# Performance work log

Hardware: AMD Instinct MI355X
Metric: run time of the kernel (lower is better)

## Reference

```python
import jax, jax.numpy as jnp
import numpy as np

B, C, H, W = 32, 256, 32, 32
IC, MC, OC = 64, 16, 256


def setup_inputs() -> dict:
    key = jax.random.key(0)
    k = jax.random.split(key, 7)
    s = 1.0 / np.sqrt(C)
    s2 = 1.0 / np.sqrt(IC * MC)
    return {
        "x": jax.random.normal(k[0], (B, C, H, W), dtype=jnp.float32),
        "info_w": jax.random.uniform(k[1], (IC, C), jnp.float32, -s, s),
        "info_b": jax.random.uniform(k[2], (IC,), jnp.float32, -s, s),
        "mask_w": jax.random.uniform(k[3], (MC, C), jnp.float32, -s, s),
        "mask_b": jax.random.uniform(k[4], (MC,), jnp.float32, -s, s),
        "out_w": jax.random.uniform(k[5], (OC, IC * MC), jnp.float32, -s2, s2),
        "out_b": jax.random.uniform(k[6], (OC,), jnp.float32, -s2, s2),
    }


def reference(x, info_w, info_b, mask_w, mask_b, out_w, out_b):
    # 1x1 convs are channel GEMMs
    info = jax.nn.relu(jnp.einsum('ic,bchw->bihw', info_w, x) + info_b[None, :, None, None])   # [B,IC,H,W]
    mask = jax.nn.sigmoid(jnp.einsum('mc,bchw->bmhw', mask_w, x) + mask_b[None, :, None, None])  # [B,MC,H,W]
    # outer product over channels; concat order = for m: info * mask[m] -> index m*IC + i
    expanded = (mask[:, :, None, :, :] * info[:, None, :, :, :]).reshape(x.shape[0], MC * IC, x.shape[2], x.shape[3])
    out = jax.nn.relu(jnp.einsum('oe,behw->bohw', out_w, expanded) + out_b[None, :, None, None])
    return out
```

## Files before the change

kernel.cpp:

```cpp
#include <hip/hip_runtime.h>


typedef short bf16x8 __attribute__((ext_vector_type(8)));
typedef float f32x4  __attribute__((ext_vector_type(4)));

#define C_   256
#define HW_  1024
#define IC_  64
#define MC_  16
#define OC_  256
#define PX_  64
#define K_   1024

__global__ __launch_bounds__(256)
void split_w(const float2* __restrict__ w2, uint4* __restrict__ dst)
{
    const int tid  = blockIdx.x * 256 + threadIdx.x;
    const int lane = tid & 63;
    const int mi   = (tid >> 6) & 1;
    const int pl   = (tid >> 7) & 1;
    const int t    = (tid >> 8) & 31;
    const int ob   = (tid >> 13) & 7;

    const int row = ob * 32 + mi * 16 + (lane & 15);
    const int kq  = t * 16 + (lane >> 4) * 4;
    const float2* src = w2 + (size_t)row * (K_ / 2) + kq;

    unsigned int o[4];
    #pragma unroll
    for (int j = 0; j < 4; ++j) {
        const float2 v = src[j];
        const unsigned int u0 = __float_as_uint(v.x);
        const unsigned int u1 = __float_as_uint(v.y);
        if (pl == 0) {
            o[j] = (u0 >> 16) | (u1 & 0xffff0000u);
        } else {
            const float r0 = v.x - __uint_as_float(u0 & 0xffff0000u);
            const float r1 = v.y - __uint_as_float(u1 & 0xffff0000u);
            o[j] = (__float_as_uint(r0) >> 16) | (__float_as_uint(r1) & 0xffff0000u);
        }
    }
    dst[tid] = make_uint4(o[0], o[1], o[2], o[3]);
}

__global__ __launch_bounds__(512, 2)
void mul_layer_kernel(const float* __restrict__ x,
                      const float* __restrict__ info_w,
                      const float* __restrict__ info_b,
                      const float* __restrict__ mask_w,
                      const float* __restrict__ mask_b,
                      const bf16x8* __restrict__ wfrag,
                      const float* __restrict__ out_b,
                      float* __restrict__ out)
{
    __shared__ unsigned short ib[2 * PX_ * IC_];
    __shared__ float mask_pk[MC_ * PX_];

    const int lane = threadIdx.x & 63;
    const int wv   = __builtin_amdgcn_readfirstlane(threadIdx.x >> 6);
    const int bimg = blockIdx.x >> 4;
    const int tile = blockIdx.x & 15;
    const int hw0  = tile * PX_;

    {
        const float* xp = x + (size_t)bimg * C_ * HW_ + hw0 + lane;
        float racc[8] = {0.f,0.f,0.f,0.f,0.f,0.f,0.f,0.f};
        float macc[2] = {0.f,0.f};

        #pragma unroll 1
        for (int c0 = 0; c0 < C_; c0 += 16) {
            float xa[16];
            #pragma unroll
            for (int j = 0; j < 16; ++j) xa[j] = xp[(size_t)(c0 + j) * HW_];
            #pragma unroll
            for (int r = 0; r < 8; ++r) {
                const float* wr_ = info_w + (wv * 8 + r) * C_ + c0;
                #pragma unroll
                for (int j = 0; j < 16; ++j) racc[r] = fmaf(wr_[j], xa[j], racc[r]);
            }
            #pragma unroll
            for (int r = 0; r < 2; ++r) {
                const float* wr_ = mask_w + (wv * 2 + r) * C_ + c0;
                #pragma unroll
                for (int j = 0; j < 16; ++j) macc[r] = fmaf(wr_[j], xa[j], macc[r]);
            }
        }

        unsigned int H[4], L[4];
        #pragma unroll
        for (int rp = 0; rp < 4; ++rp) {
            float v0 = racc[2*rp]   + info_b[wv*8 + 2*rp];
            float v1 = racc[2*rp+1] + info_b[wv*8 + 2*rp+1];
            v0 = v0 > 0.f ? v0 : 0.f;
            v1 = v1 > 0.f ? v1 : 0.f;
            const unsigned int u0 = __float_as_uint(v0);
            const unsigned int u1 = __float_as_uint(v1);
            H[rp] = (u0 >> 16) | (u1 & 0xffff0000u);
            const float r0 = v0 - __uint_as_float(u0 & 0xffff0000u);
            const float r1 = v1 - __uint_as_float(u1 & 0xffff0000u);
            L[rp] = (__float_as_uint(r0) >> 16) | (__float_as_uint(r1) & 0xffff0000u);
        }
        const int sidx = ((lane >> 4) * 2 + (wv >> 2)) * 512 + (wv & 3) * 128 + (lane & 15) * 8;
        *(uint4*)(ib + sidx)                  = make_uint4(H[0], H[1], H[2], H[3]);
        *(uint4*)(ib + (PX_ * IC_) + sidx)    = make_uint4(L[0], L[1], L[2], L[3]);

        #pragma unroll
        for (int r = 0; r < 2; ++r) {
            float z = macc[r] + mask_b[wv * 2 + r];
            mask_pk[(wv * 2 + r) * PX_ + lane] = 1.0f / (1.0f + expf(-z));
        }
    }
    __syncthreads();

    const int lr = lane & 15;
    const int lg = lane >> 4;

    const bf16x8* Bp = (const bf16x8*)((const char*)ib + lg * 256 + lr * 16);
    const float*  Mp = mask_pk + lr;
    const bf16x8* Ap = wfrag + (size_t)wv * 8192 + lane;

    f32x4 acc[2][4];
    #pragma unroll
    for (int mi = 0; mi < 2; ++mi)
        #pragma unroll
        for (int ni = 0; ni < 4; ++ni)
            acc[mi][ni] = (f32x4){0.f, 0.f, 0.f, 0.f};

    bf16x8 h0a, h0b, l0a, l0b, h1a, h1b, l1a, l1b;
    h0a = Ap[0];   h0b = Ap[64];
    l0a = Ap[128]; l0b = Ap[192];

    #pragma unroll 1
    for (int m = 0; m < MC_; ++m) {
        const int t1 = 2 * m + 1;
        h1a = Ap[t1 * 256];       h1b = Ap[t1 * 256 + 64];
        l1a = Ap[t1 * 256 + 128]; l1b = Ap[t1 * 256 + 192];

        f32x4 tmp[2][4];
        #pragma unroll
        for (int mi = 0; mi < 2; ++mi)
            #pragma unroll
            for (int ni = 0; ni < 4; ++ni)
                tmp[mi][ni] = (f32x4){0.f, 0.f, 0.f, 0.f};

        #pragma unroll
        for (int ni = 0; ni < 4; ++ni) {
            const bf16x8 Bh = Bp[(ni * 2 + 0) * 64];
            const bf16x8 Bl = Bp[512 + (ni * 2 + 0) * 64];
            tmp[0][ni] = __builtin_amdgcn_mfma_f32_16x16x32_bf16(l0a, Bh, tmp[0][ni], 0, 0, 0);
            tmp[0][ni] = __builtin_amdgcn_mfma_f32_16x16x32_bf16(h0a, Bl, tmp[0][ni], 0, 0, 0);
            tmp[0][ni] = __builtin_amdgcn_mfma_f32_16x16x32_bf16(h0a, Bh, tmp[0][ni], 0, 0, 0);
            tmp[1][ni] = __builtin_amdgcn_mfma_f32_16x16x32_bf16(l0b, Bh, tmp[1][ni], 0, 0, 0);
            tmp[1][ni] = __builtin_amdgcn_mfma_f32_16x16x32_bf16(h0b, Bl, tmp[1][ni], 0, 0, 0);
            tmp[1][ni] = __builtin_amdgcn_mfma_f32_16x16x32_bf16(h0b, Bh, tmp[1][ni], 0, 0, 0);
        }

        if (m < MC_ - 1) {
            const int t2 = 2 * m + 2;
            h0a = Ap[t2 * 256];       h0b = Ap[t2 * 256 + 64];
            l0a = Ap[t2 * 256 + 128]; l0b = Ap[t2 * 256 + 192];
        }

        #pragma unroll
        for (int ni = 0; ni < 4; ++ni) {
            const bf16x8 Bh = Bp[(ni * 2 + 1) * 64];
            const bf16x8 Bl = Bp[512 + (ni * 2 + 1) * 64];
            tmp[0][ni] = __builtin_amdgcn_mfma_f32_16x16x32_bf16(l1a, Bh, tmp[0][ni], 0, 0, 0);
            tmp[0][ni] = __builtin_amdgcn_mfma_f32_16x16x32_bf16(h1a, Bl, tmp[0][ni], 0, 0, 0);
            tmp[0][ni] = __builtin_amdgcn_mfma_f32_16x16x32_bf16(h1a, Bh, tmp[0][ni], 0, 0, 0);
            tmp[1][ni] = __builtin_amdgcn_mfma_f32_16x16x32_bf16(l1b, Bh, tmp[1][ni], 0, 0, 0);
            tmp[1][ni] = __builtin_amdgcn_mfma_f32_16x16x32_bf16(h1b, Bl, tmp[1][ni], 0, 0, 0);
            tmp[1][ni] = __builtin_amdgcn_mfma_f32_16x16x32_bf16(h1b, Bh, tmp[1][ni], 0, 0, 0);
        }

        #pragma unroll
        for (int ni = 0; ni < 4; ++ni) {
            const float mk = Mp[m * 64 + ni * 16];
            #pragma unroll
            for (int mi = 0; mi < 2; ++mi)
                #pragma unroll
                for (int q = 0; q < 4; ++q)
                    acc[mi][ni][q] = fmaf(mk, tmp[mi][ni][q], acc[mi][ni][q]);
        }
    }

    float* obase = out + (size_t)bimg * OC_ * HW_ + hw0;
    #pragma unroll
    for (int mi = 0; mi < 2; ++mi) {
        #pragma unroll
        for (int q = 0; q < 4; ++q) {
            const int oc = wv * 32 + mi * 16 + lg * 4 + q;
            const float bias = out_b[oc];
            #pragma unroll
            for (int ni = 0; ni < 4; ++ni) {
                const float v = acc[mi][ni][q] + bias;
                obase[(size_t)oc * HW_ + ni * 16 + lr] = v > 0.f ? v : 0.f;
            }
        }
    }
}

extern "C" void kernel_launch(void* const* d_in, const int* in_sizes, int n_in,
                              void* d_out, int out_size, void* d_ws, size_t ws_size,
                              hipStream_t stream) {
    const float* x      = (const float*)d_in[0];
    const float* info_w = (const float*)d_in[1];
    const float* info_b = (const float*)d_in[2];
    const float* mask_w = (const float*)d_in[3];
    const float* mask_b = (const float*)d_in[4];
    const float* out_w  = (const float*)d_in[5];
    const float* out_b  = (const float*)d_in[6];
    float* out = (float*)d_out;

    uint4* wfrag = (uint4*)d_ws;
    hipLaunchKernelGGL(split_w, dim3(256), dim3(256), 0, stream,
                       (const float2*)out_w, wfrag);

    hipLaunchKernelGGL(mul_layer_kernel, dim3(512), dim3(512), 0, stream,
                       x, info_w, info_b, mask_w, mask_b,
                       (const bf16x8*)d_ws, out_b, out);
}
```

Before: 192.3 us.

## Hoist LDS B fragments into registers and double-buffer weight fragments per mask channel

The info-activation B fragments (hi/lo bf16 split) are loaded from shared memory once into registers, since they are identical for every mask channel. This removes the repeated LDS reads inside the m loop. The loop now processes two mask channels per iteration, with a full register buffer of 8 weight fragments prefetched ahead of each compute block. Per-ni temporaries replace the 2x4 tmp array. The cost is much higher register pressure: 16 B fragments plus 16 A fragments. Under launch_bounds(512,2) this risks spills or reduced occupancy.

```diff
diff --git a/kernel.cpp b/kernel.cpp
--- a/kernel.cpp
+++ b/kernel.cpp
@@ -115,7 +115,16 @@
     const int lr = lane & 15;
     const int lg = lane >> 4;
 
-    const bf16x8* Bp = (const bf16x8*)((const char*)ib + lg * 256 + lr * 16);
+    const char* ibb = (const char*)ib + lg * 256 + lr * 16;
+    bf16x8 Bh[4][2], Bl[4][2];
+    #pragma unroll
+    for (int ni = 0; ni < 4; ++ni)
+        #pragma unroll
+        for (int kh = 0; kh < 2; ++kh) {
+            Bh[ni][kh] = *(const bf16x8*)(ibb + (ni * 2 + kh) * 1024);
+            Bl[ni][kh] = *(const bf16x8*)(ibb + 8192 + (ni * 2 + kh) * 1024);
+        }
+
     const float*  Mp = mask_pk + lr;
     const bf16x8* Ap = wfrag + (size_t)wv * 8192 + lane;
 
@@ -126,63 +135,47 @@
         for (int ni = 0; ni < 4; ++ni)
             acc[mi][ni] = (f32x4){0.f, 0.f, 0.f, 0.f};
 
-    bf16x8 h0a, h0b, l0a, l0b, h1a, h1b, l1a, l1b;
-    h0a = Ap[0];   h0b = Ap[64];
-    l0a = Ap[128]; l0b = Ap[192];
+    bf16x8 Aa[8], Ab[8];
+    #pragma unroll
+    for (int f = 0; f < 8; ++f) Aa[f] = Ap[f * 64];
+
+#define COMPUTE(mm, AB)                                                              \
+    {                                                                                \
+        _Pragma("unroll")                                                            \
+        for (int ni = 0; ni < 4; ++ni) {                                             \
+            f32x4 t0 = {0.f, 0.f, 0.f, 0.f};                                         \
+            f32x4 t1 = {0.f, 0.f, 0.f, 0.f};                                         \
+            _Pragma("unroll")                                                        \
+            for (int kh = 0; kh < 2; ++kh) {                                         \
+                t0 = __builtin_amdgcn_mfma_f32_16x16x32_bf16(AB[kh*4+2], Bh[ni][kh], t0, 0, 0, 0); \
+                t0 = __builtin_amdgcn_mfma_f32_16x16x32_bf16(AB[kh*4+0], Bl[ni][kh], t0, 0, 0, 0); \
+                t0 = __builtin_amdgcn_mfma_f32_16x16x32_bf16(AB[kh*4+0], Bh[ni][kh], t0, 0, 0, 0); \
+                t1 = __builtin_amdgcn_mfma_f32_16x16x32_bf16(AB[kh*4+3], Bh[ni][kh], t1, 0, 0, 0); \
+                t1 = __builtin_amdgcn_mfma_f32_16x16x32_bf16(AB[kh*4+1], Bl[ni][kh], t1, 0, 0, 0); \
+                t1 = __builtin_amdgcn_mfma_f32_16x16x32_bf16(AB[kh*4+1], Bh[ni][kh], t1, 0, 0, 0); \
+            }                                                                        \
+            const float mk = Mp[(mm) * 64 + ni * 16];                                \
+            _Pragma("unroll")                                                        \
+            for (int q = 0; q < 4; ++q) {                                            \
+                acc[0][ni][q] = fmaf(mk, t0[q], acc[0][ni][q]);                      \
+                acc[1][ni][q] = fmaf(mk, t1[q], acc[1][ni][q]);                      \
+            }                                                                        \
+        }                                                                            \
+    }
 
     #pragma unroll 1
-    for (int m = 0; m < MC_; ++m) {
-        const int t1 = 2 * m + 1;
-        h1a = Ap[t1 * 256];       h1b = Ap[t1 * 256 + 64];
-        l1a = Ap[t1 * 256 + 128]; l1b = Ap[t1 * 256 + 192];
-
-        f32x4 tmp[2][4];
-        #pragma unroll
-        for (int mi = 0; mi < 2; ++mi)
-            #pragma unroll
-            for (int ni = 0; ni < 4; ++ni)
-                tmp[mi][ni] = (f32x4){0.f, 0.f, 0.f, 0.f};
-
-        #pragma unroll
-        for (int ni = 0; ni < 4; ++ni) {
-            const bf16x8 Bh = Bp[(ni * 2 + 0) * 64];
-            const bf16x8 Bl = Bp[512 + (ni * 2 + 0) * 64];
-            tmp[0][ni] = __builtin_amdgcn_mfma_f32_16x16x32_bf16(l0a, Bh, tmp[0][ni], 0, 0, 0);
-            tmp[0][ni] = __builtin_amdgcn_mfma_f32_16x16x32_bf16(h0a, Bl, tmp[0][ni], 0, 0, 0);
-            tmp[0][ni] = __builtin_amdgcn_mfma_f32_16x16x32_bf16(h0a, Bh, tmp[0][ni], 0, 0, 0);
-            tmp[1][ni] = __builtin_amdgcn_mfma_f32_16x16x32_bf16(l0b, Bh, tmp[1][ni], 0, 0, 0);
-            tmp[1][ni] = __builtin_amdgcn_mfma_f32_16x16x32_bf16(h0b, Bl, tmp[1][ni], 0, 0, 0);
-            tmp[1][ni] = __builtin_amdgcn_mfma_f32_16x16x32_bf16(h0b, Bh, tmp[1][ni], 0, 0, 0);
-        }
-
-        if (m < MC_ - 1) {
-            const int t2 = 2 * m + 2;
-            h0a = Ap[t2 * 256];       h0b = Ap[t2 * 256 + 64];
-            l0a = Ap[t2 * 256 + 128]; l0b = Ap[t2 * 256 + 192];
-        }
-
-        #pragma unroll
-        for (int ni = 0; ni < 4; ++ni) {
-            const bf16x8 Bh = Bp[(ni * 2 + 1) * 64];
-            const bf16x8 Bl = Bp[512 + (ni * 2 + 1) * 64];
-            tmp[0][ni] = __builtin_amdgcn_mfma_f32_16x16x32_bf16(l1a, Bh, tmp[0][ni], 0, 0, 0);
-            tmp[0][ni] = __builtin_amdgcn_mfma_f32_16x16x32_bf16(h1a, Bl, tmp[0][ni], 0, 0, 0);
-            tmp[0][ni] = __builtin_amdgcn_mfma_f32_16x16x32_bf16(h1a, Bh, tmp[0][ni], 0, 0, 0);
-            tmp[1][ni] = __builtin_amdgcn_mfma_f32_16x16x32_bf16(l1b, Bh, tmp[1][ni], 0, 0, 0);
-            tmp[1][ni] = __builtin_amdgcn_mfma_f32_16x16x32_bf16(h1b, Bl, tmp[1][ni], 0, 0, 0);
-            tmp[1][ni] = __builtin_amdgcn_mfma_f32_16x16x32_bf16(h1b, Bh, tmp[1][ni], 0, 0, 0);
-        }
-
-        #pragma unroll
-        for (int ni = 0; ni < 4; ++ni) {
-            const float mk = Mp[m * 64 + ni * 16];
-            #pragma unroll
-            for (int mi = 0; mi < 2; ++mi)
-                #pragma unroll
-                for (int q = 0; q < 4; ++q)
-                    acc[mi][ni][q] = fmaf(mk, tmp[mi][ni][q], acc[mi][ni][q]);
-        }
-    }
+    for (int mp = 0; mp < 8; ++mp) {
+        const int m1 = 2 * mp + 1;
+        #pragma unroll
+        for (int f = 0; f < 8; ++f) Ab[f] = Ap[m1 * 512 + f * 64];
+        COMPUTE(2 * mp, Aa);
+        if (mp < 7) {
+            #pragma unroll
+            for (int f = 0; f < 8; ++f) Aa[f] = Ap[(m1 + 1) * 512 + f * 64];
+        }
+        COMPUTE(m1, Ab);
+    }
+#undef COMPUTE
 
     float* obase = out + (size_t)bimg * OC_ * HW_ + hw0;
     #pragma unroll
```

Result: faster. 187.6 us (-2.4%).

## Split fused kernel into two phases through workspace to double grid parallelism

Applied to the files above, without the earlier changes.

The single fused kernel is replaced, when the workspace is at least 11 MiB, by two kernels. The first computes info (as split hi/lo bf16) and the sigmoid mask into global workspace using 1024 blocks of 256 threads. The second runs the MFMA GEMM with 1024 blocks of 256 threads, each holding its B fragments in registers. The aim is to raise occupancy and block count over the 512 large blocks and to prefetch x in the phase-1 loop. In exchange it adds an extra launch and a round trip of the intermediates through global memory, and falls back to the fused path if the workspace is smaller.

```diff
diff --git a/kernel.cpp b/kernel.cpp
--- a/kernel.cpp
+++ b/kernel.cpp
@@ -9,8 +9,17 @@
 #define IC_  64
 #define MC_  16
 #define OC_  256
-#define PX_  64
 #define K_   1024
+
+#define WS_NEED (11u << 20)
+
+__device__ inline void split2(float v0, float v1, unsigned int& h, unsigned int& l) {
+    const unsigned int u0 = __float_as_uint(v0), u1 = __float_as_uint(v1);
+    h = (u0 >> 16) | (u1 & 0xffff0000u);
+    const float r0 = v0 - __uint_as_float(u0 & 0xffff0000u);
+    const float r1 = v1 - __uint_as_float(u1 & 0xffff0000u);
+    l = (__float_as_uint(r0) >> 16) | (__float_as_uint(r1) & 0xffff0000u);
+}
 
 __global__ __launch_bounds__(256)
 void split_w(const float2* __restrict__ w2, uint4* __restrict__ dst)
@@ -30,43 +39,198 @@
     #pragma unroll
     for (int j = 0; j < 4; ++j) {
         const float2 v = src[j];
-        const unsigned int u0 = __float_as_uint(v.x);
-        const unsigned int u1 = __float_as_uint(v.y);
-        if (pl == 0) {
-            o[j] = (u0 >> 16) | (u1 & 0xffff0000u);
-        } else {
-            const float r0 = v.x - __uint_as_float(u0 & 0xffff0000u);
-            const float r1 = v.y - __uint_as_float(u1 & 0xffff0000u);
-            o[j] = (__float_as_uint(r0) >> 16) | (__float_as_uint(r1) & 0xffff0000u);
-        }
+        unsigned int h, l;
+        split2(v.x, v.y, h, l);
+        o[j] = pl == 0 ? h : l;
     }
     dst[tid] = make_uint4(o[0], o[1], o[2], o[3]);
 }
 
+__global__ __launch_bounds__(256, 4)
+void phase1_kernel(const float* __restrict__ x,
+                   const float* __restrict__ info_w,
+                   const float* __restrict__ info_b,
+                   const float* __restrict__ mask_w,
+                   const float* __restrict__ mask_b,
+                   unsigned short* __restrict__ info_ws,
+                   float* __restrict__ mask_ws)
+{
+    const int lane = threadIdx.x & 63;
+    const int wv   = __builtin_amdgcn_readfirstlane(threadIdx.x >> 6);
+    const int tile = blockIdx.x & 511;
+    const int h    = blockIdx.x >> 9;
+    const int bimg = tile >> 4;
+    const int hw0  = (tile & 15) * 64;
+
+    const float* xp  = x + (size_t)bimg * (C_ * HW_) + hw0 + lane;
+    const float* iwr = info_w + (h * 32 + wv * 8) * C_;
+    const float* mwr = mask_w + (h * 8 + wv * 2) * C_;
+
+    float racc[8] = {0.f,0.f,0.f,0.f,0.f,0.f,0.f,0.f};
+    float macc[2] = {0.f,0.f};
+    float xa[16], xb[16];
+
+    #pragma unroll
+    for (int j = 0; j < 16; ++j) xa[j] = xp[(size_t)j * HW_];
+
+    #pragma unroll 1
+    for (int c0 = 0; c0 < C_; c0 += 32) {
+        #pragma unroll
+        for (int j = 0; j < 16; ++j) xb[j] = xp[(size_t)(c0 + 16 + j) * HW_];
+        #pragma unroll
+        for (int r = 0; r < 8; ++r) {
+            const float* w = iwr + r * C_ + c0;
+            #pragma unroll
+            for (int j = 0; j < 16; ++j) racc[r] = fmaf(w[j], xa[j], racc[r]);
+        }
+        #pragma unroll
+        for (int r = 0; r < 2; ++r) {
+            const float* w = mwr + r * C_ + c0;
+            #pragma unroll
+            for (int j = 0; j < 16; ++j) macc[r] = fmaf(w[j], xa[j], macc[r]);
+        }
+        if (c0 + 32 < C_) {
+            #pragma unroll
+            for (int j = 0; j < 16; ++j) xa[j] = xp[(size_t)(c0 + 32 + j) * HW_];
+        }
+        #pragma unroll
+        for (int r = 0; r < 8; ++r) {
+            const float* w = iwr + r * C_ + c0 + 16;
+            #pragma unroll
+            for (int j = 0; j < 16; ++j) racc[r] = fmaf(w[j], xb[j], racc[r]);
+        }
+        #pragma unroll
+        for (int r = 0; r < 2; ++r) {
+            const float* w = mwr + r * C_ + c0 + 16;
+            #pragma unroll
+            for (int j = 0; j < 16; ++j) macc[r] = fmaf(w[j], xb[j], macc[r]);
+        }
+    }
+
+    unsigned int H[4], L[4];
+    #pragma unroll
+    for (int rp = 0; rp < 4; ++rp) {
+        float v0 = racc[2*rp]   + info_b[h*32 + wv*8 + 2*rp];
+        float v1 = racc[2*rp+1] + info_b[h*32 + wv*8 + 2*rp+1];
+        v0 = v0 > 0.f ? v0 : 0.f;
+        v1 = v1 > 0.f ? v1 : 0.f;
+        split2(v0, v1, H[rp], L[rp]);
+    }
+    unsigned short* tb = info_ws + (size_t)tile * 8192;
+    const int sidx = ((lane >> 4) * 2 + h) * 512 + wv * 128 + (lane & 15) * 8;
+    *(uint4*)(tb + sidx)        = make_uint4(H[0], H[1], H[2], H[3]);
+    *(uint4*)(tb + 4096 + sidx) = make_uint4(L[0], L[1], L[2], L[3]);
+
+    #pragma unroll
+    for (int r = 0; r < 2; ++r) {
+        const float z = macc[r] + mask_b[h*8 + wv*2 + r];
+        mask_ws[(size_t)tile * 1024 + (h*8 + wv*2 + r) * 64 + lane] =
+            1.0f / (1.0f + expf(-z));
+    }
+}
+
+__global__ __launch_bounds__(256, 3)
+void phase2_kernel(const bf16x8* __restrict__ wfrag,
+                   const unsigned short* __restrict__ info_ws,
+                   const float* __restrict__ mask_ws,
+                   const float* __restrict__ out_b,
+                   float* __restrict__ out)
+{
+    const int lane = threadIdx.x & 63;
+    const int wv   = __builtin_amdgcn_readfirstlane(threadIdx.x >> 6);
+    const int tile = blockIdx.x & 511;
+    const int oh   = blockIdx.x >> 9;
+    const int q    = oh * 4 + wv;
+    const int bimg = tile >> 4;
+    const int hw0  = (tile & 15) * 64;
+    const int lr = lane & 15, lg = lane >> 4;
+
+    const char* ibb = (const char*)(info_ws + (size_t)tile * 8192) + lg * 256 + lr * 16;
+    bf16x8 Bh[4][2], Bl[4][2];
+    #pragma unroll
+    for (int ni = 0; ni < 4; ++ni)
+        #pragma unroll
+        for (int kh = 0; kh < 2; ++kh) {
+            Bh[ni][kh] = *(const bf16x8*)(ibb + (ni * 2 + kh) * 1024);
+            Bl[ni][kh] = *(const bf16x8*)(ibb + 8192 + (ni * 2 + kh) * 1024);
+        }
+
+    const float*  Mp = mask_ws + (size_t)tile * 1024 + lr;
+    const bf16x8* Ap = wfrag + (size_t)q * 8192 + lane;
+
+    f32x4 acc[2][4];
+    #pragma unroll
+    for (int mi = 0; mi < 2; ++mi)
+        #pragma unroll
+        for (int ni = 0; ni < 4; ++ni)
+            acc[mi][ni] = (f32x4){0.f, 0.f, 0.f, 0.f};
+
+    #pragma unroll 1
+    for (int m = 0; m < MC_; ++m) {
+        bf16x8 A[8];
+        #pragma unroll
+        for (int f = 0; f < 8; ++f) A[f] = Ap[m * 512 + f * 64];
+        #pragma unroll
+        for (int ni = 0; ni < 4; ++ni) {
+            f32x4 t0 = {0.f, 0.f, 0.f, 0.f};
+            f32x4 t1 = {0.f, 0.f, 0.f, 0.f};
+            #pragma unroll
+            for (int kh = 0; kh < 2; ++kh) {
+                t0 = __builtin_amdgcn_mfma_f32_16x16x32_bf16(A[kh*4+2], Bh[ni][kh], t0, 0, 0, 0);
+                t0 = __builtin_amdgcn_mfma_f32_16x16x32_bf16(A[kh*4+0], Bl[ni][kh], t0, 0, 0, 0);
+                t0 = __builtin_amdgcn_mfma_f32_16x16x32_bf16(A[kh*4+0], Bh[ni][kh], t0, 0, 0, 0);
+                t1 = __builtin_amdgcn_mfma_f32_16x16x32_bf16(A[kh*4+3], Bh[ni][kh], t1, 0, 0, 0);
+                t1 = __builtin_amdgcn_mfma_f32_16x16x32_bf16(A[kh*4+1], Bl[ni][kh], t1, 0, 0, 0);
+                t1 = __builtin_amdgcn_mfma_f32_16x16x32_bf16(A[kh*4+1], Bh[ni][kh], t1, 0, 0, 0);
+            }
+            const float mk = Mp[m * 64 + ni * 16];
+            #pragma unroll
+            for (int qq = 0; qq < 4; ++qq) {
+                acc[0][ni][qq] = fmaf(mk, t0[qq], acc[0][ni][qq]);
+                acc[1][ni][qq] = fmaf(mk, t1[qq], acc[1][ni][qq]);
+            }
+        }
+    }
+
+    float* obase = out + (size_t)bimg * OC_ * HW_ + hw0;
+    #pragma unroll
+    for (int mi = 0; mi < 2; ++mi) {
+        #pragma unroll
+        for (int qq = 0; qq < 4; ++qq) {
+            const int oc = q * 32 + mi * 16 + lg * 4 + qq;
+            const float bias = out_b[oc];
+            #pragma unroll
+            for (int ni = 0; ni < 4; ++ni) {
+                const float v = acc[mi][ni][qq] + bias;
+                obase[(size_t)oc * HW_ + ni * 16 + lr] = v > 0.f ? v : 0.f;
+            }
+        }
+    }
+}
+
 __global__ __launch_bounds__(512, 2)
-void mul_layer_kernel(const float* __restrict__ x,
-                      const float* __restrict__ info_w,
-                      const float* __restrict__ info_b,
-                      const float* __restrict__ mask_w,
-                      const float* __restrict__ mask_b,
-                      const bf16x8* __restrict__ wfrag,
-                      const float* __restrict__ out_b,
-                      float* __restrict__ out)
+void fused_kernel(const float* __restrict__ x,
+                  const float* __restrict__ info_w,
+                  const float* __restrict__ info_b,
+                  const float* __restrict__ mask_w,
+                  const float* __restrict__ mask_b,
+                  const bf16x8* __restrict__ wfrag,
+                  const float* __restrict__ out_b,
+                  float* __restrict__ out)
 {
-    __shared__ unsigned short ib[2 * PX_ * IC_];
-    __shared__ float mask_pk[MC_ * PX_];
+    __shared__ unsigned short ib[2 * 64 * IC_];
+    __shared__ float mask_pk[MC_ * 64];
 
     const int lane = threadIdx.x & 63;
     const int wv   = __builtin_amdgcn_readfirstlane(threadIdx.x >> 6);
     const int bimg = blockIdx.x >> 4;
     const int tile = blockIdx.x & 15;
-    const int hw0  = tile * PX_;
+    const int hw0  = tile * 64;
 
     {
         const float* xp = x + (size_t)bimg * C_ * HW_ + hw0 + lane;
         float racc[8] = {0.f,0.f,0.f,0.f,0.f,0.f,0.f,0.f};
         float macc[2] = {0.f,0.f};
-
         #pragma unroll 1
         for (int c0 = 0; c0 < C_; c0 += 16) {
             float xa[16];
@@ -85,7 +249,6 @@
                 for (int j = 0; j < 16; ++j) macc[r] = fmaf(wr_[j], xa[j], macc[r]);
             }
         }
-
         unsigned int H[4], L[4];
         #pragma unroll
         for (int rp = 0; rp < 4; ++rp) {
@@ -93,29 +256,29 @@
             float v1 = racc[2*rp+1] + info_b[wv*8 + 2*rp+1];
             v0 = v0 > 0.f ? v0 : 0.f;
             v1 = v1 > 0.f ? v1 : 0.f;
-            const unsigned int u0 = __float_as_uint(v0);
-            const unsigned int u1 = __float_as_uint(v1);
-            H[rp] = (u0 >> 16) | (u1 & 0xffff0000u);
-            const float r0 = v0 - __uint_as_float(u0 & 0xffff0000u);
-            const float r1 = v1 - __uint_as_float(u1 & 0xffff0000u);
-            L[rp] = (__float_as_uint(r0) >> 16) | (__float_as_uint(r1) & 0xffff0000u);
+            split2(v0, v1, H[rp], L[rp]);
         }
         const int sidx = ((lane >> 4) * 2 + (wv >> 2)) * 512 + (wv & 3) * 128 + (lane & 15) * 8;
-        *(uint4*)(ib + sidx)                  = make_uint4(H[0], H[1], H[2], H[3]);
-        *(uint4*)(ib + (PX_ * IC_) + sidx)    = make_uint4(L[0], L[1], L[2], L[3]);
-
+        *(uint4*)(ib + sidx)             = make_uint4(H[0], H[1], H[2], H[3]);
+        *(uint4*)(ib + 4096 + sidx)      = make_uint4(L[0], L[1], L[2], L[3]);
         #pragma unroll
         for (int r = 0; r < 2; ++r) {
             float z = macc[r] + mask_b[wv * 2 + r];
-            mask_pk[(wv * 2 + r) * PX_ + lane] = 1.0f / (1.0f + expf(-z));
+            mask_pk[(wv * 2 + r) * 64 + lane] = 1.0f / (1.0f + expf(-z));
         }
     }
     __syncthreads();
 
-    const int lr = lane & 15;
-    const int lg = lane >> 4;
-
-    const bf16x8* Bp = (const bf16x8*)((const char*)ib + lg * 256 + lr * 16);
+    const int lr = lane & 15, lg = lane >> 4;
+    const char* ibb = (const char*)ib + lg * 256 + lr * 16;
+    bf16x8 Bh[4][2], Bl[4][2];
+    #pragma unroll
+    for (int ni = 0; ni < 4; ++ni)
+        #pragma unroll
+        for (int kh = 0; kh < 2; ++kh) {
+            Bh[ni][kh] = *(const bf16x8*)(ibb + (ni * 2 + kh) * 1024);
+            Bl[ni][kh] = *(const bf16x8*)(ibb + 8192 + (ni * 2 + kh) * 1024);
+        }
     const float*  Mp = mask_pk + lr;
     const bf16x8* Ap = wfrag + (size_t)wv * 8192 + lane;
 
@@ -126,61 +289,30 @@
         for (int ni = 0; ni < 4; ++ni)
             acc[mi][ni] = (f32x4){0.f, 0.f, 0.f, 0.f};
 
-    bf16x8 h0a, h0b, l0a, l0b, h1a, h1b, l1a, l1b;
-    h0a = Ap[0];   h0b = Ap[64];
-    l0a = Ap[128]; l0b = Ap[192];
-
     #pragma unroll 1
     for (int m = 0; m < MC_; ++m) {
-        const int t1 = 2 * m + 1;
-        h1a = Ap[t1 * 256];       h1b = Ap[t1 * 256 + 64];
-        l1a = Ap[t1 * 256 + 128]; l1b = Ap[t1 * 256 + 192];
-
-        f32x4 tmp[2][4];
-        #pragma unroll
-        for (int mi = 0; mi < 2; ++mi)
-            #pragma unroll
-            for (int ni = 0; ni < 4; ++ni)
-                tmp[mi][ni] = (f32x4){0.f, 0.f, 0.f, 0.f};
-
+        bf16x8 A[8];
+        #pragma unroll
+        for (int f = 0; f < 8; ++f) A[f] = Ap[m * 512 + f * 64];
         #pragma unroll
         for (int ni = 0; ni < 4; ++ni) {
-            const bf16x8 Bh = Bp[(ni * 2 + 0) * 64];
-            const bf16x8 Bl = Bp[512 + (ni * 2 + 0) * 64];
-            tmp[0][ni] = __builtin_amdgcn_mfma_f32_16x16x32_bf16(l0a, Bh, tmp[0][ni], 0, 0, 0);
-            tmp[0][ni] = __builtin_amdgcn_mfma_f32_16x16x32_bf16(h0a, Bl, tmp[0][ni], 0, 0, 0);
-            tmp[0][ni] = __builtin_amdgcn_mfma_f32_16x16x32_bf16(h0a, Bh, tmp[0][ni], 0, 0, 0);
-            tmp[1][ni] = __builtin_amdgcn_mfma_f32_16x16x32_bf16(l0b, Bh, tmp[1][ni], 0, 0, 0);
-            tmp[1][ni] = __builtin_amdgcn_mfma_f32_16x16x32_bf16(h0b, Bl, tmp[1][ni], 0, 0, 0);
-            tmp[1][ni] = __builtin_amdgcn_mfma_f32_16x16x32_bf16(h0b, Bh, tmp[1][ni], 0, 0, 0);
-        }
-
-        if (m < MC_ - 1) {
-            const int t2 = 2 * m + 2;
-            h0a = Ap[t2 * 256];       h0b = Ap[t2 * 256 + 64];
-            l0a = Ap[t2 * 256 + 128]; l0b = Ap[t2 * 256 + 192];
-        }
-
-        #pragma unroll
-        for (int ni = 0; ni < 4; ++ni) {
-            const bf16x8 Bh = Bp[(ni * 2 + 1) * 64];
-            const bf16x8 Bl = Bp[512 + (ni * 2 + 1) * 64];
-            tmp[0][ni] = __builtin_amdgcn_mfma_f32_16x16x32_bf16(l1a, Bh, tmp[0][ni], 0, 0, 0);
-            tmp[0][ni] = __builtin_amdgcn_mfma_f32_16x16x32_bf16(h1a, Bl, tmp[0][ni], 0, 0, 0);
-            tmp[0][ni] = __builtin_amdgcn_mfma_f32_16x16x32_bf16(h1a, Bh, tmp[0][ni], 0, 0, 0);
-            tmp[1][ni] = __builtin_amdgcn_mfma_f32_16x16x32_bf16(l1b, Bh, tmp[1][ni], 0, 0, 0);
-            tmp[1][ni] = __builtin_amdgcn_mfma_f32_16x16x32_bf16(h1b, Bl, tmp[1][ni], 0, 0, 0);
-            tmp[1][ni] = __builtin_amdgcn_mfma_f32_16x16x32_bf16(h1b, Bh, tmp[1][ni], 0, 0, 0);
-        }
-
-        #pragma unroll
-        for (int ni = 0; ni < 4; ++ni) {
+            f32x4 t0 = {0.f,0.f,0.f,0.f};
+            f32x4 t1 = {0.f,0.f,0.f,0.f};
+            #pragma unroll
+            for (int kh = 0; kh < 2; ++kh) {
+                t0 = __builtin_amdgcn_mfma_f32_16x16x32_bf16(A[kh*4+2], Bh[ni][kh], t0, 0, 0, 0);
+                t0 = __builtin_amdgcn_mfma_f32_16x16x32_bf16(A[kh*4+0], Bl[ni][kh], t0, 0, 0, 0);
+                t0 = __builtin_amdgcn_mfma_f32_16x16x32_bf16(A[kh*4+0], Bh[ni][kh], t0, 0, 0, 0);
+                t1 = __builtin_amdgcn_mfma_f32_16x16x32_bf16(A[kh*4+3], Bh[ni][kh], t1, 0, 0, 0);
+                t1 = __builtin_amdgcn_mfma_f32_16x16x32_bf16(A[kh*4+1], Bl[ni][kh], t1, 0, 0, 0);
+                t1 = __builtin_amdgcn_mfma_f32_16x16x32_bf16(A[kh*4+1], Bh[ni][kh], t1, 0, 0, 0);
+            }
             const float mk = Mp[m * 64 + ni * 16];
             #pragma unroll
-            for (int mi = 0; mi < 2; ++mi)
-                #pragma unroll
-                for (int q = 0; q < 4; ++q)
-                    acc[mi][ni][q] = fmaf(mk, tmp[mi][ni][q], acc[mi][ni][q]);
+            for (int qq = 0; qq < 4; ++qq) {
+                acc[0][ni][qq] = fmaf(mk, t0[qq], acc[0][ni][qq]);
+                acc[1][ni][qq] = fmaf(mk, t1[qq], acc[1][ni][qq]);
+            }
         }
     }
 
@@ -188,12 +320,12 @@
     #pragma unroll
     for (int mi = 0; mi < 2; ++mi) {
         #pragma unroll
-        for (int q = 0; q < 4; ++q) {
-            const int oc = wv * 32 + mi * 16 + lg * 4 + q;
+        for (int qq = 0; qq < 4; ++qq) {
+            const int oc = wv * 32 + mi * 16 + lg * 4 + qq;
             const float bias = out_b[oc];
             #pragma unroll
             for (int ni = 0; ni < 4; ++ni) {
-                const float v = acc[mi][ni][q] + bias;
+                const float v = acc[mi][ni][qq] + bias;
                 obase[(size_t)oc * HW_ + ni * 16 + lr] = v > 0.f ? v : 0.f;
             }
         }
@@ -216,7 +348,16 @@
     hipLaunchKernelGGL(split_w, dim3(256), dim3(256), 0, stream,
                        (const float2*)out_w, wfrag);
 
-    hipLaunchKernelGGL(mul_layer_kernel, dim3(512), dim3(512), 0, stream,
-                       x, info_w, info_b, mask_w, mask_b,
-                       (const bf16x8*)d_ws, out_b, out);
-}
+    if (ws_size >= WS_NEED) {
+        unsigned short* info_ws = (unsigned short*)((char*)d_ws + (1u << 20));
+        float*          mask_ws = (float*)((char*)d_ws + (9u << 20));
+        hipLaunchKernelGGL(phase1_kernel, dim3(1024), dim3(256), 0, stream,
+                           x, info_w, info_b, mask_w, mask_b, info_ws, mask_ws);
+        hipLaunchKernelGGL(phase2_kernel, dim3(1024), dim3(256), 0, stream,
+                           (const bf16x8*)d_ws, info_ws, mask_ws, out_b, out);
+    } else {
+        hipLaunchKernelGGL(fused_kernel, dim3(512), dim3(512), 0, stream,
+                           x, info_w, info_b, mask_w, mask_b,
+                           (const bf16x8*)d_ws, out_b, out);
+    }
+}
```

Result: faster. 167.6 us (-12.8%).
